# Kernel tuning notes

Hardware: AMD Instinct MI355X
Metric: run time of the kernel (lower is better)

## Reference

```python
import jax, jax.numpy as jnp
import numpy as np

B, C1, C2, K, S, HDIM = 8, 16, 16, 3, 1, 16
H = W = 64


def setup_inputs() -> dict:
    key = jax.random.key(0)
    k0, k1, k2 = jax.random.split(key, 3)
    x = jax.random.normal(k0, (B, C1, H, W), jnp.float32)
    # torch.nn.Linear default init scale ~ 1/sqrt(fan_in)
    fc1_w = jax.random.normal(k1, (HDIM, 5), jnp.float32) * (1.0 / np.sqrt(5.0))
    fc1_b = jnp.zeros((HDIM,), jnp.float32)
    fc2_w = jax.random.normal(k2, (C2 * C1 * K * K, HDIM), jnp.float32) * (1.0 / np.sqrt(HDIM))
    fc2_b = jnp.zeros((C2 * C1 * K * K,), jnp.float32)
    return {"x": x, "fc1_w": fc1_w, "fc1_b": fc1_b, "fc2_w": fc2_w, "fc2_b": fc2_b}


def _unfold_same(x, k, s):
    """F.pad('same'-style) + F.unfold. Returns (patches [B, L, C*k*k], out_h, out_w).
    Channel ordering matches torch unfold: index = c*k*k + i*k + j (channel-major)."""
    Bq, C, Hq, Wq = x.shape
    out_h = (Hq + s - 1) // s
    out_w = (Wq + s - 1) // s
    pad_h = max((out_h - 1) * s + k - Hq, 0)
    pad_w = max((out_w - 1) * s + k - Wq, 0)
    pt, pb = pad_h // 2, pad_h - pad_h // 2
    pl, pr = pad_w // 2, pad_w - pad_w // 2
    xp = jnp.pad(x, ((0, 0), (0, 0), (pt, pb), (pl, pr)))
    # k*k shifted views; loop over tiny fixed k*k=9 taps only
    cols = jnp.stack(
        [xp[:, :, i:i + out_h * s:s, j:j + out_w * s:s] for i in range(k) for j in range(k)],
        axis=2,
    )  # [B, C, k*k, out_h, out_w]
    patches = cols.reshape(Bq, C * k * k, out_h * out_w).transpose(0, 2, 1)  # [B, L, C*k*k]
    return patches, out_h, out_w


def reference(x, fc1_w, fc1_b, fc2_w, fc2_b):
    patches, oh, ow = _unfold_same(x, K, S)  # [B, L, N] with N = C1*K*K
    Bq, L, N = patches.shape
    mu = patches.mean(-1, keepdims=True)
    # torch.std default is unbiased (ddof=1)
    var = jnp.sum((patches - mu) ** 2, axis=-1, keepdims=True) / (N - 1)
    sigma = jnp.sqrt(var) + 1e-6
    normed = (patches - mu) / sigma
    skew = jnp.mean(normed ** 3, axis=-1, keepdims=True)
    kurt = jnp.mean(normed ** 4, axis=-1, keepdims=True) - 3.0
    prob = jax.nn.softmax(patches, axis=-1)
    entropy = -jnp.sum(prob * jnp.log(prob + 1e-6), axis=-1, keepdims=True)
    stats = jnp.concatenate([mu, sigma, skew, kurt, entropy], axis=-1)  # [B, L, 5]
    stats = jax.lax.stop_gradient(stats)  # .detach() in the original
    h = jax.nn.relu(stats @ fc1_w.T + fc1_b)                 # [B, L, hdim]
    weights = (h @ fc2_w.T + fc2_b).reshape(Bq, L, C2, N)    # [B, L, c2, c1*k*k]
    out = jnp.einsum('blco,blo->blc', weights, patches)      # per-location dynamic conv
    return out.transpose(0, 2, 1).reshape(Bq, C2, oh, ow)
```

## Files before the change

kernel.cpp:

```cpp
#include <hip/hip_runtime.h>
#include <math.h>


typedef __attribute__((ext_vector_type(8))) short short8;
typedef __attribute__((ext_vector_type(4))) float float4v;

#define NPq 144

__device__ __forceinline__ unsigned short f2bf(float f) {
    unsigned int u = __builtin_bit_cast(unsigned int, f);
    u += 0x7fffu + ((u >> 16) & 1u);
    return (unsigned short)(u >> 16);
}
__device__ __forceinline__ float bf2f(unsigned short h) {
    unsigned int u = ((unsigned int)h) << 16;
    return __builtin_bit_cast(float, u);
}

__global__ void prep_bfrag(const float* __restrict__ fc2_w,
                           const float* __restrict__ fc2_b,
                           unsigned short* __restrict__ Bfrag) {
    const int blk  = blockIdx.x;
    const int t    = blk / 5, s = blk % 5;
    const int lane = threadIdx.x;
    const int n    = lane & 15, q = lane >> 4;
    short8 v;
#pragma unroll
    for (int j = 0; j < 8; ++j) {
        const int k = s * 32 + q * 8 + j;
        float w = 0.f;
        if (k < NPq) w = (t < 16) ? fc2_w[(t * NPq + k) * 16 + n]
                                  : fc2_b[n * NPq + k];
        v[j] = (short)f2bf(w);
    }
    *(short8*)(Bfrag + (size_t)(blk * 64 + lane) * 8) = v;
}

__global__ __launch_bounds__(256, 2) void sacconv_kernel(
    const float* __restrict__ x,
    const float* __restrict__ fc1_w,
    const float* __restrict__ fc1_b,
    const unsigned short* __restrict__ Bfrag,
    float* __restrict__ out)
{
    __shared__ unsigned short SH[64 * 280];
    __shared__ float redA[4][64];
    __shared__ float redB[4][64];
    __shared__ float redC[4][64];
    __shared__ float redD[4][64];
    __shared__ float sb[64][8];
    __shared__ float Hl[64][20];

    const int t   = threadIdx.x;
    const int blk = blockIdx.x;
    const int b   = blk >> 6;
    const int y   = blk & 63;

    const int loc = t & 63;
    const int grp = t >> 6;
    const int mt  = loc >> 4;

    float v[36];
    {
        const int thrbase = mt * 2560 + (loc & 15) * 8;
        float s = 0.f, mx = -1e30f;
#pragma unroll
        for (int i = 0; i < 36; ++i) {
            const int c1 = grp * 4 + i / 9;
            const int ii = (i % 9) / 3;
            const int jj = i % 3;
            const int yy = y + ii - 1;
            const int xx = loc + jj - 1;
            float val = 0.f;
            if (yy >= 0 && yy < 64 && xx >= 0 && xx < 64)
                val = x[((b * 16 + c1) * 64 + yy) * 64 + xx];
            v[i] = val;
            const int o = grp * 36 + i;
            SH[thrbase + (o >> 5) * 512 + ((o >> 3) & 3) * 128 + (o & 7)] = f2bf(val);
            s += val;
            mx = fmaxf(mx, val);
        }
        redA[grp][loc] = s;
        redB[grp][loc] = mx;
        const int idx = t & 63;
        unsigned short* zp = &SH[((grp * 5 + 4) * 64 + 32) * 8 + idx * 4];
        *(uint2*)zp = make_uint2(0u, 0u);
    }
    __syncthreads();
    if (t < 64) {
        float s  = redA[0][t] + redA[1][t] + redA[2][t] + redA[3][t];
        float mx = fmaxf(fmaxf(redB[0][t], redB[1][t]), fmaxf(redB[2][t], redB[3][t]));
        sb[t][0] = s * (1.f / 144.f);
        sb[t][1] = mx;
    }
    __syncthreads();

    {
        const float mu = sb[loc][0], mx = sb[loc][1];
        float m2 = 0.f, m3 = 0.f, m4 = 0.f, se = 0.f;
#pragma unroll
        for (int i = 0; i < 36; ++i) {
            const float d  = v[i] - mu;
            const float d2 = d * d;
            m2 += d2; m3 += d2 * d; m4 += d2 * d2;
            se += __expf(v[i] - mx);
        }
        redA[grp][loc] = m2; redB[grp][loc] = m3;
        redC[grp][loc] = m4; redD[grp][loc] = se;
    }
    __syncthreads();
    if (t < 64) {
        float m2 = redA[0][t] + redA[1][t] + redA[2][t] + redA[3][t];
        float m3 = redB[0][t] + redB[1][t] + redB[2][t] + redB[3][t];
        float m4 = redC[0][t] + redC[1][t] + redC[2][t] + redC[3][t];
        float Z  = redD[0][t] + redD[1][t] + redD[2][t] + redD[3][t];
        float var   = m2 * (1.f / 143.f);
        float sigma = sqrtf(var) + 1e-6f;
        float is  = 1.f / sigma;
        float is2 = is * is;
        sb[t][2] = sigma;
        sb[t][3] = (m3 * (1.f / 144.f)) * is2 * is;
        sb[t][4] = (m4 * (1.f / 144.f)) * is2 * is2 - 3.f;
        sb[t][5] = 1.f / Z;
    }
    __syncthreads();

    {
        const float mx = sb[loc][1], invZ = sb[loc][5];
        float ent = 0.f;
#pragma unroll
        for (int i = 0; i < 36; ++i) {
            const float pr = __expf(v[i] - mx) * invZ;
            ent += pr * __logf(pr + 1e-6f);
        }
        redA[grp][loc] = ent;
    }
    __syncthreads();

    {
        const float ent = -(redA[0][loc] + redA[1][loc] + redA[2][loc] + redA[3][loc]);
        const float s0 = sb[loc][0], s1 = sb[loc][2], s2 = sb[loc][3], s3 = sb[loc][4];
#pragma unroll
        for (int j0 = 0; j0 < 4; ++j0) {
            const int j = grp * 4 + j0;
            const float* wr = fc1_w + j * 5;
            float hv = s0 * wr[0] + s1 * wr[1] + s2 * wr[2] + s3 * wr[3]
                     + ent * wr[4] + fc1_b[j];
            Hl[loc][j] = fmaxf(hv, 0.f);
        }
    }

    const int w    = __builtin_amdgcn_readfirstlane(t >> 6);
    const int lane = t & 63;

    short8 af[5];
#pragma unroll
    for (int s = 0; s < 5; ++s)
        af[s] = *(const short8*)&SH[((w * 5 + s) * 64 + lane) * 8];

    float4v acc[17];
#pragma unroll
    for (int tt = 0; tt < 17; ++tt) acc[tt] = (float4v){0.f, 0.f, 0.f, 0.f};

    const short8* Bf = (const short8*)Bfrag;
    short8 cur[5], nxt[5];
#pragma unroll
    for (int s = 0; s < 5; ++s) cur[s] = Bf[s * 64 + lane];

#pragma unroll
    for (int tt = 0; tt < 17; ++tt) {
        if (tt < 16) {
#pragma unroll
            for (int s = 0; s < 5; ++s) nxt[s] = Bf[((tt + 1) * 5 + s) * 64 + lane];
        }
#pragma unroll
        for (int s = 0; s < 5; ++s)
            acc[tt] = __builtin_amdgcn_mfma_f32_16x16x32_bf16(af[s], cur[s], acc[tt], 0, 0, 0);
        if (tt < 16) {
#pragma unroll
            for (int s = 0; s < 5; ++s) cur[s] = nxt[s];
        }
    }

    __syncthreads();
    {
        const int nn = lane & 15, qq = lane >> 4;
#pragma unroll
        for (int tt = 0; tt < 17; ++tt) {
            const int col = tt * 16 + nn;
#pragma unroll
            for (int r = 0; r < 4; ++r) {
                const int row = w * 16 + qq * 4 + r;
                SH[row * 280 + col] = f2bf(acc[tt][r]);
            }
        }
    }
    __syncthreads();

    {
        float hv[16];
#pragma unroll
        for (int j = 0; j < 16; ++j) hv[j] = Hl[loc][j];
        const int cg = w * 4;
#pragma unroll
        for (int cc = 0; cc < 4; ++cc) {
            const int c = cg + cc;
            const unsigned short* qr = &SH[loc * 280 + c * 16];
            short8 q0 = *(const short8*)qr;
            short8 q1 = *(const short8*)(qr + 8);
            float res = bf2f(SH[loc * 280 + 256 + c]);
#pragma unroll
            for (int j = 0; j < 8; ++j) res += hv[j]     * bf2f((unsigned short)q0[j]);
#pragma unroll
            for (int j = 0; j < 8; ++j) res += hv[8 + j] * bf2f((unsigned short)q1[j]);
            out[(b * 16 + c) * 4096 + y * 64 + loc] = res;
        }
    }
}

extern "C" void kernel_launch(void* const* d_in, const int* in_sizes, int n_in,
                              void* d_out, int out_size, void* d_ws, size_t ws_size,
                              hipStream_t stream) {
    const float* x     = (const float*)d_in[0];
    const float* fc1_w = (const float*)d_in[1];
    const float* fc1_b = (const float*)d_in[2];
    const float* fc2_w = (const float*)d_in[3];
    const float* fc2_b = (const float*)d_in[4];
    float* out = (float*)d_out;
    unsigned short* Bfrag = (unsigned short*)d_ws;

    prep_bfrag<<<85, 64, 0, stream>>>(fc2_w, fc2_b, Bfrag);
    sacconv_kernel<<<512, 256, 0, stream>>>(x, fc1_w, fc1_b, Bfrag, out);
}
```

Before: 81.13 us.

## Split MFMA work across waves by N-tile and pack A-fragment LDS stores

Each wave previously ran all 17 N-tiles against its own 16-row M-tile, so every wave loaded the full Bfrag from global memory. Now each wave loads the whole A matrix from LDS and computes only its share of N-tiles (4 tiles, plus the bias tile on wave 3). This cuts global Bfrag traffic per wave by about four times. The patch gather is also restructured so each thread writes packed short8 chunks to LDS instead of scalar stores, giving threads uneven loads of 40 or 32 values. In exchange, register pressure rises (20 A fragments and 20 accumulators) and wave 3 does extra work.

New measurement: 87.56 us. 1.08x slower.

```diff
diff --git a/kernel.cpp b/kernel.cpp
--- a/kernel.cpp
+++ b/kernel.cpp
@@ -59,31 +59,40 @@
     const int loc = t & 63;
     const int grp = t >> 6;
     const int mt  = loc >> 4;
-
-    float v[36];
-    {
-        const int thrbase = mt * 2560 + (loc & 15) * 8;
+    const int m   = loc & 15;
+
+    const int nchunk = (grp < 2) ? 5 : 4;
+    const int nv     = nchunk * 8;
+
+    float v[40];
+    {
         float s = 0.f, mx = -1e30f;
 #pragma unroll
-        for (int i = 0; i < 36; ++i) {
-            const int c1 = grp * 4 + i / 9;
-            const int ii = (i % 9) / 3;
-            const int jj = i % 3;
-            const int yy = y + ii - 1;
-            const int xx = loc + jj - 1;
-            float val = 0.f;
-            if (yy >= 0 && yy < 64 && xx >= 0 && xx < 64)
-                val = x[((b * 16 + c1) * 64 + yy) * 64 + xx];
-            v[i] = val;
-            const int o = grp * 36 + i;
-            SH[thrbase + (o >> 5) * 512 + ((o >> 3) & 3) * 128 + (o & 7)] = f2bf(val);
-            s += val;
-            mx = fmaxf(mx, val);
+        for (int u = 0; u < 5; ++u) {
+            if (u >= nchunk) break;
+            const int c = grp + 4 * u;
+            short8 pk;
+#pragma unroll
+            for (int j = 0; j < 8; ++j) {
+                const int o  = c * 8 + j;
+                const int c1 = o / 9;
+                const int ii = (o % 9) / 3;
+                const int jj = o % 3;
+                const int yy = y + ii - 1;
+                const int xx = loc + jj - 1;
+                float val = 0.f;
+                if (yy >= 0 && yy < 64 && xx >= 0 && xx < 64)
+                    val = x[((b * 16 + c1) * 64 + yy) * 64 + xx];
+                v[u * 8 + j] = val;
+                pk[j] = (short)f2bf(val);
+                s += val;
+                mx = fmaxf(mx, val);
+            }
+            *(short8*)&SH[mt * 2560 + (c >> 2) * 512 + (c & 3) * 128 + m * 8] = pk;
         }
         redA[grp][loc] = s;
         redB[grp][loc] = mx;
-        const int idx = t & 63;
-        unsigned short* zp = &SH[((grp * 5 + 4) * 64 + 32) * 8 + idx * 4];
+        unsigned short* zp = &SH[((grp * 5 + 4) * 64 + 32) * 8 + loc * 4];
         *(uint2*)zp = make_uint2(0u, 0u);
     }
     __syncthreads();
@@ -99,7 +108,8 @@
         const float mu = sb[loc][0], mx = sb[loc][1];
         float m2 = 0.f, m3 = 0.f, m4 = 0.f, se = 0.f;
 #pragma unroll
-        for (int i = 0; i < 36; ++i) {
+        for (int i = 0; i < 40; ++i) {
+            if (i >= nv) break;
             const float d  = v[i] - mu;
             const float d2 = d * d;
             m2 += d2; m3 += d2 * d; m4 += d2 * d2;
@@ -129,7 +139,8 @@
         const float mx = sb[loc][1], invZ = sb[loc][5];
         float ent = 0.f;
 #pragma unroll
-        for (int i = 0; i < 36; ++i) {
+        for (int i = 0; i < 40; ++i) {
+            if (i >= nv) break;
             const float pr = __expf(v[i] - mx) * invZ;
             ent += pr * __logf(pr + 1e-6f);
         }
@@ -153,46 +164,68 @@
     const int w    = __builtin_amdgcn_readfirstlane(t >> 6);
     const int lane = t & 63;
 
-    short8 af[5];
-#pragma unroll
-    for (int s = 0; s < 5; ++s)
-        af[s] = *(const short8*)&SH[((w * 5 + s) * 64 + lane) * 8];
-
-    float4v acc[17];
-#pragma unroll
-    for (int tt = 0; tt < 17; ++tt) acc[tt] = (float4v){0.f, 0.f, 0.f, 0.f};
+    short8 af[4][5];
+#pragma unroll
+    for (int mm = 0; mm < 4; ++mm)
+#pragma unroll
+        for (int s = 0; s < 5; ++s)
+            af[mm][s] = *(const short8*)&SH[((mm * 5 + s) * 64 + lane) * 8];
+
+    float4v acc[20];
+#pragma unroll
+    for (int i = 0; i < 20; ++i) acc[i] = (float4v){0.f, 0.f, 0.f, 0.f};
 
     const short8* Bf = (const short8*)Bfrag;
-    short8 cur[5], nxt[5];
-#pragma unroll
-    for (int s = 0; s < 5; ++s) cur[s] = Bf[s * 64 + lane];
-
-#pragma unroll
-    for (int tt = 0; tt < 17; ++tt) {
-        if (tt < 16) {
-#pragma unroll
-            for (int s = 0; s < 5; ++s) nxt[s] = Bf[((tt + 1) * 5 + s) * 64 + lane];
-        }
-#pragma unroll
-        for (int s = 0; s < 5; ++s)
-            acc[tt] = __builtin_amdgcn_mfma_f32_16x16x32_bf16(af[s], cur[s], acc[tt], 0, 0, 0);
-        if (tt < 16) {
-#pragma unroll
-            for (int s = 0; s < 5; ++s) cur[s] = nxt[s];
-        }
+    short8 bcur[5], bnxt[5];
+#pragma unroll
+    for (int s = 0; s < 5; ++s) bcur[s] = Bf[(w * 5 + s) * 64 + lane];
+
+#pragma unroll
+    for (int u = 0; u < 4; ++u) {
+        if (u < 3) {
+            const int tn = w + 4 * (u + 1);
+#pragma unroll
+            for (int s = 0; s < 5; ++s) bnxt[s] = Bf[(tn * 5 + s) * 64 + lane];
+        } else if (w == 3) {
+#pragma unroll
+            for (int s = 0; s < 5; ++s) bnxt[s] = Bf[(16 * 5 + s) * 64 + lane];
+        }
+#pragma unroll
+        for (int mm = 0; mm < 4; ++mm)
+#pragma unroll
+            for (int s = 0; s < 5; ++s)
+                acc[u * 4 + mm] = __builtin_amdgcn_mfma_f32_16x16x32_bf16(
+                    af[mm][s], bcur[s], acc[u * 4 + mm], 0, 0, 0);
+#pragma unroll
+        for (int s = 0; s < 5; ++s) bcur[s] = bnxt[s];
+    }
+    if (w == 3) {
+#pragma unroll
+        for (int mm = 0; mm < 4; ++mm)
+#pragma unroll
+            for (int s = 0; s < 5; ++s)
+                acc[16 + mm] = __builtin_amdgcn_mfma_f32_16x16x32_bf16(
+                    af[mm][s], bcur[s], acc[16 + mm], 0, 0, 0);
     }
 
     __syncthreads();
     {
         const int nn = lane & 15, qq = lane >> 4;
 #pragma unroll
-        for (int tt = 0; tt < 17; ++tt) {
-            const int col = tt * 16 + nn;
-#pragma unroll
-            for (int r = 0; r < 4; ++r) {
-                const int row = w * 16 + qq * 4 + r;
-                SH[row * 280 + col] = f2bf(acc[tt][r]);
-            }
+        for (int u = 0; u < 4; ++u) {
+            const int colb = (w + 4 * u) * 16 + nn;
+#pragma unroll
+            for (int mm = 0; mm < 4; ++mm)
+#pragma unroll
+                for (int r = 0; r < 4; ++r)
+                    SH[(mm * 16 + qq * 4 + r) * 280 + colb] = f2bf(acc[u * 4 + mm][r]);
+        }
+        if (w == 3) {
+#pragma unroll
+            for (int mm = 0; mm < 4; ++mm)
+#pragma unroll
+                for (int r = 0; r < 4; ++r)
+                    SH[(mm * 16 + qq * 4 + r) * 280 + 256 + nn] = f2bf(acc[16 + mm][r]);
         }
     }
     __syncthreads();
```

## Use closed-form softmax entropy, pack LDS stores, and retile MFMA as 2x9 per wave

Applied to the files above, without the earlier changes.

Entropy is now computed in closed form as log Z + max - sum(e*v)/Z, accumulated in the same pass as the moments. This removes a second exp/log pass over the 36 values and two block barriers, at the cost of dropping the 1e-6 epsilon inside the log. The bf16 patch writes to LDS are packed four at a time into 8-byte stores. The MFMA work is retiled so each wave covers two M-tiles and nine N-tiles, which halves per-wave fragment loads of the fc2 weights but adds one redundant overlapping N-tile. Small LDS arrays are padded to reduce bank conflicts.

Result: faster. 74.63 us (-8.0%).

```diff
diff --git a/kernel.cpp b/kernel.cpp
--- a/kernel.cpp
+++ b/kernel.cpp
@@ -48,8 +48,9 @@
     __shared__ float redB[4][64];
     __shared__ float redC[4][64];
     __shared__ float redD[4][64];
-    __shared__ float sb[64][8];
-    __shared__ float Hl[64][20];
+    __shared__ float redE[4][64];
+    __shared__ float sb[64][9];
+    __shared__ float Hl[64][21];
 
     const int t   = threadIdx.x;
     const int blk = blockIdx.x;
@@ -59,31 +60,42 @@
     const int loc = t & 63;
     const int grp = t >> 6;
     const int mt  = loc >> 4;
+    const int m   = loc & 15;
 
     float v[36];
     {
-        const int thrbase = mt * 2560 + (loc & 15) * 8;
         float s = 0.f, mx = -1e30f;
 #pragma unroll
-        for (int i = 0; i < 36; ++i) {
-            const int c1 = grp * 4 + i / 9;
-            const int ii = (i % 9) / 3;
-            const int jj = i % 3;
-            const int yy = y + ii - 1;
-            const int xx = loc + jj - 1;
-            float val = 0.f;
-            if (yy >= 0 && yy < 64 && xx >= 0 && xx < 64)
-                val = x[((b * 16 + c1) * 64 + yy) * 64 + xx];
-            v[i] = val;
-            const int o = grp * 36 + i;
-            SH[thrbase + (o >> 5) * 512 + ((o >> 3) & 3) * 128 + (o & 7)] = f2bf(val);
-            s += val;
-            mx = fmaxf(mx, val);
+        for (int u = 0; u < 9; ++u) {
+            const int c = grp + 4 * u;
+            unsigned int lo, hi;
+#pragma unroll
+            for (int d = 0; d < 4; ++d) {
+                const int o  = c * 4 + d;
+                const int c1 = o / 9;
+                const int ii = (o % 9) / 3;
+                const int jj = o % 3;
+                const int yy = y + ii - 1;
+                const int xx = loc + jj - 1;
+                float val = 0.f;
+                if (yy >= 0 && yy < 64 && xx >= 0 && xx < 64)
+                    val = x[((b * 16 + c1) * 64 + yy) * 64 + xx];
+                v[u * 4 + d] = val;
+                s += val;
+                mx = fmaxf(mx, val);
+                const unsigned int bf = f2bf(val);
+                if (d == 0) lo = bf;
+                else if (d == 1) lo |= bf << 16;
+                else if (d == 2) hi = bf;
+                else hi |= bf << 16;
+            }
+            unsigned short* dst = &SH[mt * 2560 + (c >> 3) * 512 + ((c >> 1) & 3) * 128
+                                      + m * 8 + (c & 1) * 4];
+            *(uint2*)dst = make_uint2(lo, hi);
         }
         redA[grp][loc] = s;
         redB[grp][loc] = mx;
-        const int idx = t & 63;
-        unsigned short* zp = &SH[((grp * 5 + 4) * 64 + 32) * 8 + idx * 4];
+        unsigned short* zp = &SH[((grp * 5 + 4) * 64 + 32) * 8 + loc * 4];
         *(uint2*)zp = make_uint2(0u, 0u);
     }
     __syncthreads();
@@ -91,22 +103,24 @@
         float s  = redA[0][t] + redA[1][t] + redA[2][t] + redA[3][t];
         float mx = fmaxf(fmaxf(redB[0][t], redB[1][t]), fmaxf(redB[2][t], redB[3][t]));
         sb[t][0] = s * (1.f / 144.f);
-        sb[t][1] = mx;
-    }
-    __syncthreads();
-
-    {
-        const float mu = sb[loc][0], mx = sb[loc][1];
-        float m2 = 0.f, m3 = 0.f, m4 = 0.f, se = 0.f;
+        sb[t][5] = mx;
+    }
+    __syncthreads();
+
+    {
+        const float mu = sb[loc][0], mx = sb[loc][5];
+        float m2 = 0.f, m3 = 0.f, m4 = 0.f, se = 0.f, sev = 0.f;
 #pragma unroll
         for (int i = 0; i < 36; ++i) {
             const float d  = v[i] - mu;
             const float d2 = d * d;
             m2 += d2; m3 += d2 * d; m4 += d2 * d2;
-            se += __expf(v[i] - mx);
+            const float e = __expf(v[i] - mx);
+            se += e; sev += e * v[i];
         }
         redA[grp][loc] = m2; redB[grp][loc] = m3;
         redC[grp][loc] = m4; redD[grp][loc] = se;
+        redE[grp][loc] = sev;
     }
     __syncthreads();
     if (t < 64) {
@@ -114,71 +128,68 @@
         float m3 = redB[0][t] + redB[1][t] + redB[2][t] + redB[3][t];
         float m4 = redC[0][t] + redC[1][t] + redC[2][t] + redC[3][t];
         float Z  = redD[0][t] + redD[1][t] + redD[2][t] + redD[3][t];
+        float S  = redE[0][t] + redE[1][t] + redE[2][t] + redE[3][t];
         float var   = m2 * (1.f / 143.f);
         float sigma = sqrtf(var) + 1e-6f;
         float is  = 1.f / sigma;
         float is2 = is * is;
-        sb[t][2] = sigma;
-        sb[t][3] = (m3 * (1.f / 144.f)) * is2 * is;
-        sb[t][4] = (m4 * (1.f / 144.f)) * is2 * is2 - 3.f;
-        sb[t][5] = 1.f / Z;
-    }
-    __syncthreads();
-
-    {
-        const float mx = sb[loc][1], invZ = sb[loc][5];
-        float ent = 0.f;
-#pragma unroll
-        for (int i = 0; i < 36; ++i) {
-            const float pr = __expf(v[i] - mx) * invZ;
-            ent += pr * __logf(pr + 1e-6f);
-        }
-        redA[grp][loc] = ent;
-    }
-    __syncthreads();
-
-    {
-        const float ent = -(redA[0][loc] + redA[1][loc] + redA[2][loc] + redA[3][loc]);
-        const float s0 = sb[loc][0], s1 = sb[loc][2], s2 = sb[loc][3], s3 = sb[loc][4];
+        sb[t][1] = sigma;
+        sb[t][2] = (m3 * (1.f / 144.f)) * is2 * is;
+        sb[t][3] = (m4 * (1.f / 144.f)) * is2 * is2 - 3.f;
+        sb[t][4] = __logf(Z) + sb[t][5] - S / Z;
+    }
+    __syncthreads();
+
+    {
+        const float s0 = sb[loc][0], s1 = sb[loc][1], s2 = sb[loc][2],
+                    s3 = sb[loc][3], s4 = sb[loc][4];
 #pragma unroll
         for (int j0 = 0; j0 < 4; ++j0) {
             const int j = grp * 4 + j0;
             const float* wr = fc1_w + j * 5;
             float hv = s0 * wr[0] + s1 * wr[1] + s2 * wr[2] + s3 * wr[3]
-                     + ent * wr[4] + fc1_b[j];
+                     + s4 * wr[4] + fc1_b[j];
             Hl[loc][j] = fmaxf(hv, 0.f);
         }
     }
 
     const int w    = __builtin_amdgcn_readfirstlane(t >> 6);
+    const int mp   = w >> 1;
+    const int nh   = w & 1;
+    const int nb   = nh * 8;
     const int lane = t & 63;
 
-    short8 af[5];
-#pragma unroll
-    for (int s = 0; s < 5; ++s)
-        af[s] = *(const short8*)&SH[((w * 5 + s) * 64 + lane) * 8];
-
-    float4v acc[17];
-#pragma unroll
-    for (int tt = 0; tt < 17; ++tt) acc[tt] = (float4v){0.f, 0.f, 0.f, 0.f};
+    short8 af[2][5];
+#pragma unroll
+    for (int mm = 0; mm < 2; ++mm)
+#pragma unroll
+        for (int s = 0; s < 5; ++s)
+            af[mm][s] = *(const short8*)&SH[((2 * mp + mm) * 5 + s) * 512 + lane * 8];
+
+    float4v acc[18];
+#pragma unroll
+    for (int i = 0; i < 18; ++i) acc[i] = (float4v){0.f, 0.f, 0.f, 0.f};
 
     const short8* Bf = (const short8*)Bfrag;
-    short8 cur[5], nxt[5];
-#pragma unroll
-    for (int s = 0; s < 5; ++s) cur[s] = Bf[s * 64 + lane];
-
-#pragma unroll
-    for (int tt = 0; tt < 17; ++tt) {
-        if (tt < 16) {
-#pragma unroll
-            for (int s = 0; s < 5; ++s) nxt[s] = Bf[((tt + 1) * 5 + s) * 64 + lane];
-        }
-#pragma unroll
-        for (int s = 0; s < 5; ++s)
-            acc[tt] = __builtin_amdgcn_mfma_f32_16x16x32_bf16(af[s], cur[s], acc[tt], 0, 0, 0);
-        if (tt < 16) {
-#pragma unroll
-            for (int s = 0; s < 5; ++s) cur[s] = nxt[s];
+    short8 bcur[5], bnxt[5];
+#pragma unroll
+    for (int s = 0; s < 5; ++s) bcur[s] = Bf[((nb) * 5 + s) * 64 + lane];
+
+#pragma unroll
+    for (int u = 0; u < 9; ++u) {
+        if (u < 8) {
+#pragma unroll
+            for (int s = 0; s < 5; ++s) bnxt[s] = Bf[((nb + u + 1) * 5 + s) * 64 + lane];
+        }
+#pragma unroll
+        for (int mm = 0; mm < 2; ++mm)
+#pragma unroll
+            for (int s = 0; s < 5; ++s)
+                acc[u * 2 + mm] = __builtin_amdgcn_mfma_f32_16x16x32_bf16(
+                    af[mm][s], bcur[s], acc[u * 2 + mm], 0, 0, 0);
+        if (u < 8) {
+#pragma unroll
+            for (int s = 0; s < 5; ++s) bcur[s] = bnxt[s];
         }
     }
 
@@ -186,12 +197,14 @@
     {
         const int nn = lane & 15, qq = lane >> 4;
 #pragma unroll
-        for (int tt = 0; tt < 17; ++tt) {
-            const int col = tt * 16 + nn;
-#pragma unroll
-            for (int r = 0; r < 4; ++r) {
-                const int row = w * 16 + qq * 4 + r;
-                SH[row * 280 + col] = f2bf(acc[tt][r]);
+        for (int u = 0; u < 9; ++u) {
+            const int col = (nb + u) * 16 + nn;
+#pragma unroll
+            for (int mm = 0; mm < 2; ++mm) {
+                const int rowb = (2 * mp + mm) * 16 + qq * 4;
+#pragma unroll
+                for (int r = 0; r < 4; ++r)
+                    SH[(rowb + r) * 280 + col] = f2bf(acc[u * 2 + mm][r]);
             }
         }
     }
```

## Restructure to single-wave blocks with register MFMA fragments and shuffle reductions

Applied to the files above, without the earlier changes.

Each block becomes one 64-lane wave that handles 16 pixels (2048 blocks). Each lane loads its patch slice directly into the MFMA A-fragment layout, and the per-pixel statistics are reduced with cross-lane shuffles instead of shared-memory reductions and several block barriers. Entropy now uses the closed form log Z + max − Σe·v/Z, which removes a second exp/log pass. The cost is that each block does the full Bfrag MFMA sweep for only 16 pixels instead of 64, and the closed-form entropy drops the +1e-6 inside the log.

After: 85.40 us. 1.05x slower.

```diff
diff --git a/kernel.cpp b/kernel.cpp
--- a/kernel.cpp
+++ b/kernel.cpp
@@ -36,184 +36,141 @@
     *(short8*)(Bfrag + (size_t)(blk * 64 + lane) * 8) = v;
 }
 
-__global__ __launch_bounds__(256, 2) void sacconv_kernel(
+__global__ __launch_bounds__(64, 2) void sacconv_kernel(
     const float* __restrict__ x,
     const float* __restrict__ fc1_w,
     const float* __restrict__ fc1_b,
     const unsigned short* __restrict__ Bfrag,
     float* __restrict__ out)
 {
-    __shared__ unsigned short SH[64 * 280];
-    __shared__ float redA[4][64];
-    __shared__ float redB[4][64];
-    __shared__ float redC[4][64];
-    __shared__ float redD[4][64];
-    __shared__ float sb[64][8];
-    __shared__ float Hl[64][20];
+    __shared__ unsigned short Qs[16 * 288];
 
-    const int t   = threadIdx.x;
-    const int blk = blockIdx.x;
-    const int b   = blk >> 6;
-    const int y   = blk & 63;
+    const int lane = threadIdx.x;
+    const int blk  = blockIdx.x;
+    const int b    = blk >> 8;
+    const int y    = (blk >> 2) & 63;
+    const int x0   = (blk & 3) << 4;
 
-    const int loc = t & 63;
-    const int grp = t >> 6;
-    const int mt  = loc >> 4;
+    const int m  = lane & 15;
+    const int q  = lane >> 4;
+    const int xm = x0 + m;
 
-    float v[36];
-    {
-        const int thrbase = mt * 2560 + (loc & 15) * 8;
-        float s = 0.f, mx = -1e30f;
+    float v[5][8];
+    short8 af[5];
+    float sum = 0.f, mx = -1e30f;
 #pragma unroll
-        for (int i = 0; i < 36; ++i) {
-            const int c1 = grp * 4 + i / 9;
-            const int ii = (i % 9) / 3;
-            const int jj = i % 3;
-            const int yy = y + ii - 1;
-            const int xx = loc + jj - 1;
+    for (int s = 0; s < 5; ++s) {
+#pragma unroll
+        for (int j = 0; j < 8; ++j) {
+            const int o = s * 32 + q * 8 + j;
             float val = 0.f;
-            if (yy >= 0 && yy < 64 && xx >= 0 && xx < 64)
-                val = x[((b * 16 + c1) * 64 + yy) * 64 + xx];
-            v[i] = val;
-            const int o = grp * 36 + i;
-            SH[thrbase + (o >> 5) * 512 + ((o >> 3) & 3) * 128 + (o & 7)] = f2bf(val);
-            s += val;
-            mx = fmaxf(mx, val);
-        }
-        redA[grp][loc] = s;
-        redB[grp][loc] = mx;
-        const int idx = t & 63;
-        unsigned short* zp = &SH[((grp * 5 + 4) * 64 + 32) * 8 + idx * 4];
-        *(uint2*)zp = make_uint2(0u, 0u);
-    }
-    __syncthreads();
-    if (t < 64) {
-        float s  = redA[0][t] + redA[1][t] + redA[2][t] + redA[3][t];
-        float mx = fmaxf(fmaxf(redB[0][t], redB[1][t]), fmaxf(redB[2][t], redB[3][t]));
-        sb[t][0] = s * (1.f / 144.f);
-        sb[t][1] = mx;
-    }
-    __syncthreads();
-
-    {
-        const float mu = sb[loc][0], mx = sb[loc][1];
-        float m2 = 0.f, m3 = 0.f, m4 = 0.f, se = 0.f;
-#pragma unroll
-        for (int i = 0; i < 36; ++i) {
-            const float d  = v[i] - mu;
-            const float d2 = d * d;
-            m2 += d2; m3 += d2 * d; m4 += d2 * d2;
-            se += __expf(v[i] - mx);
-        }
-        redA[grp][loc] = m2; redB[grp][loc] = m3;
-        redC[grp][loc] = m4; redD[grp][loc] = se;
-    }
-    __syncthreads();
-    if (t < 64) {
-        float m2 = redA[0][t] + redA[1][t] + redA[2][t] + redA[3][t];
-        float m3 = redB[0][t] + redB[1][t] + redB[2][t] + redB[3][t];
-        float m4 = redC[0][t] + redC[1][t] + redC[2][t] + redC[3][t];
-        float Z  = redD[0][t] + redD[1][t] + redD[2][t] + redD[3][t];
-        float var   = m2 * (1.f / 143.f);
-        float sigma = sqrtf(var) + 1e-6f;
-        float is  = 1.f / sigma;
-        float is2 = is * is;
-        sb[t][2] = sigma;
-        sb[t][3] = (m3 * (1.f / 144.f)) * is2 * is;
-        sb[t][4] = (m4 * (1.f / 144.f)) * is2 * is2 - 3.f;
-        sb[t][5] = 1.f / Z;
-    }
-    __syncthreads();
-
-    {
-        const float mx = sb[loc][1], invZ = sb[loc][5];
-        float ent = 0.f;
-#pragma unroll
-        for (int i = 0; i < 36; ++i) {
-            const float pr = __expf(v[i] - mx) * invZ;
-            ent += pr * __logf(pr + 1e-6f);
-        }
-        redA[grp][loc] = ent;
-    }
-    __syncthreads();
-
-    {
-        const float ent = -(redA[0][loc] + redA[1][loc] + redA[2][loc] + redA[3][loc]);
-        const float s0 = sb[loc][0], s1 = sb[loc][2], s2 = sb[loc][3], s3 = sb[loc][4];
-#pragma unroll
-        for (int j0 = 0; j0 < 4; ++j0) {
-            const int j = grp * 4 + j0;
-            const float* wr = fc1_w + j * 5;
-            float hv = s0 * wr[0] + s1 * wr[1] + s2 * wr[2] + s3 * wr[3]
-                     + ent * wr[4] + fc1_b[j];
-            Hl[loc][j] = fmaxf(hv, 0.f);
+            if (o < NPq) {
+                const int c1 = o / 9;
+                const int rm = o - c1 * 9;
+                const int ii = rm / 3;
+                const int jj = rm - ii * 3;
+                const int yy = y + ii - 1;
+                const int xp = xm + jj - 1;
+                if (yy >= 0 && yy < 64 && xp >= 0 && xp < 64)
+                    val = x[((b * 16 + c1) * 64 + yy) * 64 + xp];
+                sum += val;
+                mx = fmaxf(mx, val);
+            }
+            v[s][j] = val;
+            af[s][j] = (short)f2bf(val);
         }
     }
+    sum += __shfl_xor(sum, 16, 64);
+    sum += __shfl_xor(sum, 32, 64);
+    mx = fmaxf(mx, __shfl_xor(mx, 16, 64));
+    mx = fmaxf(mx, __shfl_xor(mx, 32, 64));
+    const float mu = sum * (1.f / 144.f);
 
-    const int w    = __builtin_amdgcn_readfirstlane(t >> 6);
-    const int lane = t & 63;
+    float m2 = 0.f, m3 = 0.f, m4 = 0.f, se = 0.f, sev = 0.f;
+#pragma unroll
+    for (int s = 0; s < 5; ++s) {
+#pragma unroll
+        for (int j = 0; j < 8; ++j) {
+            const int o = s * 32 + q * 8 + j;
+            if (o < NPq) {
+                const float d  = v[s][j] - mu;
+                const float d2 = d * d;
+                m2 += d2; m3 += d2 * d; m4 += d2 * d2;
+                const float e = __expf(v[s][j] - mx);
+                se += e; sev += e * v[s][j];
+            }
+        }
+    }
+    m2 += __shfl_xor(m2, 16, 64);  m2 += __shfl_xor(m2, 32, 64);
+    m3 += __shfl_xor(m3, 16, 64);  m3 += __shfl_xor(m3, 32, 64);
+    m4 += __shfl_xor(m4, 16, 64);  m4 += __shfl_xor(m4, 32, 64);
+    se += __shfl_xor(se, 16, 64);  se += __shfl_xor(se, 32, 64);
+    sev += __shfl_xor(sev, 16, 64); sev += __shfl_xor(sev, 32, 64);
 
-    short8 af[5];
-#pragma unroll
-    for (int s = 0; s < 5; ++s)
-        af[s] = *(const short8*)&SH[((w * 5 + s) * 64 + lane) * 8];
+    const float var   = m2 * (1.f / 143.f);
+    const float sigma = sqrtf(var) + 1e-6f;
+    const float is    = 1.f / sigma;
+    const float is2   = is * is;
+    const float skew  = (m3 * (1.f / 144.f)) * is2 * is;
+    const float kurt  = (m4 * (1.f / 144.f)) * is2 * is2 - 3.f;
+    const float ent   = __logf(se) + mx - sev / se;
 
     float4v acc[17];
 #pragma unroll
     for (int tt = 0; tt < 17; ++tt) acc[tt] = (float4v){0.f, 0.f, 0.f, 0.f};
 
     const short8* Bf = (const short8*)Bfrag;
-    short8 cur[5], nxt[5];
+    short8 bcur[5], bnxt[5];
 #pragma unroll
-    for (int s = 0; s < 5; ++s) cur[s] = Bf[s * 64 + lane];
+    for (int s = 0; s < 5; ++s) bcur[s] = Bf[s * 64 + lane];
 
 #pragma unroll
     for (int tt = 0; tt < 17; ++tt) {
         if (tt < 16) {
 #pragma unroll
-            for (int s = 0; s < 5; ++s) nxt[s] = Bf[((tt + 1) * 5 + s) * 64 + lane];
+            for (int s = 0; s < 5; ++s) bnxt[s] = Bf[((tt + 1) * 5 + s) * 64 + lane];
         }
 #pragma unroll
         for (int s = 0; s < 5; ++s)
-            acc[tt] = __builtin_amdgcn_mfma_f32_16x16x32_bf16(af[s], cur[s], acc[tt], 0, 0, 0);
+            acc[tt] = __builtin_amdgcn_mfma_f32_16x16x32_bf16(af[s], bcur[s], acc[tt], 0, 0, 0);
         if (tt < 16) {
 #pragma unroll
-            for (int s = 0; s < 5; ++s) cur[s] = nxt[s];
+            for (int s = 0; s < 5; ++s) bcur[s] = bnxt[s];
         }
     }
 
-    __syncthreads();
     {
         const int nn = lane & 15, qq = lane >> 4;
 #pragma unroll
         for (int tt = 0; tt < 17; ++tt) {
-            const int col = tt * 16 + nn;
 #pragma unroll
-            for (int r = 0; r < 4; ++r) {
-                const int row = w * 16 + qq * 4 + r;
-                SH[row * 280 + col] = f2bf(acc[tt][r]);
-            }
+            for (int r = 0; r < 4; ++r)
+                Qs[(qq * 4 + r) * 288 + tt * 16 + nn] = f2bf(acc[tt][r]);
         }
     }
     __syncthreads();
 
     {
-        float hv[16];
+        float h[16];
 #pragma unroll
-        for (int j = 0; j < 16; ++j) hv[j] = Hl[loc][j];
-        const int cg = w * 4;
+        for (int j = 0; j < 16; ++j) {
+            const float* wr = fc1_w + j * 5;
+            const float hv = mu * wr[0] + sigma * wr[1] + skew * wr[2]
+                           + kurt * wr[3] + ent * wr[4] + fc1_b[j];
+            h[j] = fmaxf(hv, 0.f);
+        }
 #pragma unroll
         for (int cc = 0; cc < 4; ++cc) {
-            const int c = cg + cc;
-            const unsigned short* qr = &SH[loc * 280 + c * 16];
+            const int c = q * 4 + cc;
+            const unsigned short* qr = &Qs[m * 288 + c * 16];
             short8 q0 = *(const short8*)qr;
             short8 q1 = *(const short8*)(qr + 8);
-            float res = bf2f(SH[loc * 280 + 256 + c]);
+            float res = bf2f(Qs[m * 288 + 256 + c]);
 #pragma unroll
-            for (int j = 0; j < 8; ++j) res += hv[j]     * bf2f((unsigned short)q0[j]);
+            for (int j = 0; j < 8; ++j) res += h[j]     * bf2f((unsigned short)q0[j]);
 #pragma unroll
-            for (int j = 0; j < 8; ++j) res += hv[8 + j] * bf2f((unsigned short)q1[j]);
-            out[(b * 16 + c) * 4096 + y * 64 + loc] = res;
+            for (int j = 0; j < 8; ++j) res += h[8 + j] * bf2f((unsigned short)q1[j]);
+            out[(b * 16 + c) * 4096 + y * 64 + x0 + m] = res;
         }
     }
 }
@@ -230,5 +187,5 @@
     unsigned short* Bfrag = (unsigned short*)d_ws;
 
     prep_bfrag<<<85, 64, 0, stream>>>(fc2_w, fc2_b, Bfrag);
-    sacconv_kernel<<<512, 256, 0, stream>>>(x, fc1_w, fc1_b, Bfrag, out);
+    sacconv_kernel<<<2048, 64, 0, stream>>>(x, fc1_w, fc1_b, Bfrag, out);
 }
```
